# Performance work log

Measured on AMD Instinct MI355X. Metric: run time of the kernel, lower is better.

## Reference

```python
import jax, jax.numpy as jnp
import numpy as np

SCALE, Z, X, Y = 4, 9, 9, 9
INV_SQRT_2PI = 1.0 / np.sqrt(2.0 * np.pi)


def setup_inputs() -> dict:
    key = jax.random.key(0)
    k1, = jax.random.split(key, 1)
    inp = jax.random.normal(k1, (1, 1, 128, 512, 512), dtype=jnp.float32)
    return {
        "inp": inp,
        "mu_z": jnp.asarray(0.0, dtype=jnp.float32),
        "sig_z": jnp.asarray(0.1, dtype=jnp.float32),
        "bet_xy": jnp.asarray(2.0, dtype=jnp.float32),
        "bet_z": jnp.asarray(1.5, dtype=jnp.float32),
    }


def _gen_alf(bet_xy, bet_z):
    # squared distances along each axis; torch's loop overwrites the wrap-around
    # write, so the net result for odd sizes is simply (arange - size//2)**2
    zd = ((jnp.arange(Z) - Z // 2) ** 2).astype(jnp.float32)[:, None, None]
    xd = ((jnp.arange(X) - X // 2) ** 2).astype(jnp.float32)[None, :, None]
    yd = ((jnp.arange(Y) - Y // 2) ** 2).astype(jnp.float32)[None, None, :]
    d_2 = zd / bet_z ** 2 + (xd + yd) / bet_xy ** 2  # (Z, X, Y)
    return jnp.exp(-d_2 / 2) * INV_SQRT_2PI


def reference(inp, mu_z, sig_z, bet_xy, bet_z):
    z0 = jnp.exp(mu_z + 0.5 * sig_z ** 2)
    rec = inp * z0  # (N, 1, D, H, W)
    alf = _gen_alf(bet_xy, bet_z)[None, None]  # (1, 1, Z, X, Y)
    pad_z = (Z - SCALE + 1) // 2
    rec = jax.lax.conv_general_dilated(
        rec, alf,
        window_strides=(SCALE, 1, 1),
        padding=[(pad_z, pad_z), (X // 2, X // 2), (Y // 2, Y // 2)],
        dimension_numbers=("NCDHW", "OIDHW", "NCDHW"),
    )  # (N, 1, D//SCALE, H, W)
    rec = (rec - rec.min()) / (rec.max() - rec.min())
    return rec
```

## Files before the change

kernel.cpp:

```cpp
#include <hip/hip_runtime.h>

#define D_IN  128
#define D_OUT 32
#define H     512
#define W     512
#define W4    128
#define HB    16
#define ZR    (HB + 8)
#define NTHR  512

__global__ __launch_bounds__(NTHR)
void conv3d_fused(const float* __restrict__ inp, float* __restrict__ out,
                  const float* __restrict__ bxy_p, const float* __restrict__ bz_p,
                  float* __restrict__ blkMin, float* __restrict__ blkMax) {
    __shared__ float zbuf[ZR * W];
    __shared__ float hbuf[HB * W];

    const int d  = blockIdx.x >> 5;
    const int h0 = (blockIdx.x & 31) * HB;

    const float bz = bz_p[0], bx = bxy_p[0];
    const float iz = 1.0f / (2.0f * bz * bz);
    const float ix = 1.0f / (2.0f * bx * bx);
    float wz[9], wx[9];
#pragma unroll
    for (int k = 0; k < 9; ++k) {
        float dd = (float)(k - 4);
        wz[k] = expf(-dd * dd * iz);
        wx[k] = expf(-dd * dd * ix);
    }

    const float4* in4 = (const float4*)inp;
    float4* z4 = (float4*)zbuf;
    float4* h4 = (float4*)hbuf;

    for (int t = threadIdx.x; t < ZR * W4; t += NTHR) {
        int r  = t >> 7;
        int c4 = t & (W4 - 1);
        int h  = h0 - 4 + r;
        float4 acc = make_float4(0.f, 0.f, 0.f, 0.f);
        if ((unsigned)h < H) {
            int base = h * W4 + c4;
#pragma unroll
            for (int k = 0; k < 9; ++k) {
                int din = 4 * d - 3 + k;
                if ((unsigned)din < D_IN) {
                    float4 v = in4[din * (H * W4) + base];
                    acc.x += v.x * wz[k]; acc.y += v.y * wz[k];
                    acc.z += v.z * wz[k]; acc.w += v.w * wz[k];
                }
            }
        }
        z4[t] = acc;
    }
    __syncthreads();

    for (int t = threadIdx.x; t < HB * W4; t += NTHR) {
        int r  = t >> 7;
        int c4 = t & (W4 - 1);
        float4 acc = make_float4(0.f, 0.f, 0.f, 0.f);
#pragma unroll
        for (int k = 0; k < 9; ++k) {
            float4 v = z4[(r + k) * W4 + c4];
            acc.x += v.x * wx[k]; acc.y += v.y * wx[k];
            acc.z += v.z * wx[k]; acc.w += v.w * wx[k];
        }
        h4[t] = acc;
    }
    __syncthreads();

    float lmin =  3.402823466e38f;
    float lmax = -3.402823466e38f;
    float4* out4 = (float4*)out;
    for (int t = threadIdx.x; t < HB * W4; t += NTHR) {
        int r  = t >> 7;
        int c4 = t & (W4 - 1);
        float4 zv = make_float4(0.f, 0.f, 0.f, 0.f);
        float4 va = (c4 > 0)      ? h4[r * W4 + c4 - 1] : zv;
        float4 vb =                 h4[r * W4 + c4];
        float4 vc = (c4 < W4 - 1) ? h4[r * W4 + c4 + 1] : zv;
        float win[12] = {va.x, va.y, va.z, va.w,
                         vb.x, vb.y, vb.z, vb.w,
                         vc.x, vc.y, vc.z, vc.w};
        float4 o = make_float4(0.f, 0.f, 0.f, 0.f);
#pragma unroll
        for (int k = 0; k < 9; ++k) {
            o.x += win[k]     * wx[k];
            o.y += win[k + 1] * wx[k];
            o.z += win[k + 2] * wx[k];
            o.w += win[k + 3] * wx[k];
        }
        out4[(d * H + h0 + r) * W4 + c4] = o;
        lmin = fminf(lmin, fminf(fminf(o.x, o.y), fminf(o.z, o.w)));
        lmax = fmaxf(lmax, fmaxf(fmaxf(o.x, o.y), fmaxf(o.z, o.w)));
    }

#pragma unroll
    for (int off = 32; off > 0; off >>= 1) {
        lmin = fminf(lmin, __shfl_down(lmin, off, 64));
        lmax = fmaxf(lmax, __shfl_down(lmax, off, 64));
    }
    float* smin = &zbuf[0];
    float* smax = &zbuf[16];
    int lane = threadIdx.x & 63, wv = threadIdx.x >> 6;
    if (lane == 0) { smin[wv] = lmin; smax[wv] = lmax; }
    __syncthreads();
    if (threadIdx.x == 0) {
        float mn = smin[0], mx = smax[0];
#pragma unroll
        for (int i = 1; i < 8; ++i) { mn = fminf(mn, smin[i]); mx = fmaxf(mx, smax[i]); }
        blkMin[blockIdx.x] = mn;
        blkMax[blockIdx.x] = mx;
    }
}

__global__ void reduce_kernel(const float* __restrict__ blkMin, const float* __restrict__ blkMax,
                              float* __restrict__ fin, int nblk) {
    float lmin =  3.402823466e38f;
    float lmax = -3.402823466e38f;
    for (int i = threadIdx.x; i < nblk; i += blockDim.x) {
        lmin = fminf(lmin, blkMin[i]);
        lmax = fmaxf(lmax, blkMax[i]);
    }
#pragma unroll
    for (int off = 32; off > 0; off >>= 1) {
        lmin = fminf(lmin, __shfl_down(lmin, off, 64));
        lmax = fmaxf(lmax, __shfl_down(lmax, off, 64));
    }
    __shared__ float smin[4], smax[4];
    int lane = threadIdx.x & 63, wv = threadIdx.x >> 6;
    if (lane == 0) { smin[wv] = lmin; smax[wv] = lmax; }
    __syncthreads();
    if (threadIdx.x == 0) {
        fin[0] = fminf(fminf(smin[0], smin[1]), fminf(smin[2], smin[3]));
        fin[1] = fmaxf(fmaxf(smax[0], smax[1]), fmaxf(smax[2], smax[3]));
    }
}

__global__ void norm_kernel(const float* __restrict__ in, float* __restrict__ out,
                            const float* __restrict__ fin) {
    int tid = blockIdx.x * blockDim.x + threadIdx.x;
    float mn  = fin[0];
    float inv = 1.0f / (fin[1] - mn);
    float4 v = ((const float4*)in)[tid];
    ((float4*)out)[tid] = make_float4((v.x - mn) * inv, (v.y - mn) * inv,
                                      (v.z - mn) * inv, (v.w - mn) * inv);
}

extern "C" void kernel_launch(void* const* d_in, const int* in_sizes, int n_in,
                              void* d_out, int out_size, void* d_ws, size_t ws_size,
                              hipStream_t stream) {
    const float* inp    = (const float*)d_in[0];
    const float* bet_xy = (const float*)d_in[3];
    const float* bet_z  = (const float*)d_in[4];
    float* out = (float*)d_out;

    char* ws = (char*)d_ws;
    float* fin    = (float*)ws;
    float* blkMin = (float*)(ws + 4096);
    float* blkMax = (float*)(ws + 8192);
    float* bufA   = (float*)(ws + 65536);

    const int CONV_GRID = D_OUT * (H / HB);
    conv3d_fused<<<CONV_GRID, NTHR, 0, stream>>>(inp, bufA, bet_xy, bet_z, blkMin, blkMax);
    reduce_kernel<<<1, 256, 0, stream>>>(blkMin, blkMax, fin, CONV_GRID);

    const int NTASK = D_OUT * H * W4;
    norm_kernel<<<NTASK / 256, 256, 0, stream>>>(bufA, out, fin);
}
```

Before: 242.3 us.

## Split z-convolution into its own kernel and use atomic min/max reduction

The z-axis convolution becomes a separate elementwise kernel writing an intermediate buffer, so the HW conv kernel no longer recomputes the 9-tap z sum for its 8 halo rows on every block. The block height is halved and the separate reduce kernel is replaced by order-preserving uint atomicMin/atomicMax. Costs are an extra round trip of a 32 MB intermediate through global memory and one more launch, and the halo overhead ratio rises with the smaller tile.

```diff
diff --git a/kernel.cpp b/kernel.cpp
--- a/kernel.cpp
+++ b/kernel.cpp
@@ -5,57 +5,89 @@
 #define H     512
 #define W     512
 #define W4    128
-#define HB    16
+#define HB    8
 #define ZR    (HB + 8)
-#define NTHR  512
+#define K2THR 512
 
-__global__ __launch_bounds__(NTHR)
-void conv3d_fused(const float* __restrict__ inp, float* __restrict__ out,
-                  const float* __restrict__ bxy_p, const float* __restrict__ bz_p,
-                  float* __restrict__ blkMin, float* __restrict__ blkMax) {
-    __shared__ float zbuf[ZR * W];
-    __shared__ float hbuf[HB * W];
+__device__ __forceinline__ unsigned f2key(float f) {
+    unsigned u = __float_as_uint(f);
+    return (u & 0x80000000u) ? ~u : (u | 0x80000000u);
+}
+__device__ __forceinline__ float key2f(unsigned k) {
+    unsigned u = (k & 0x80000000u) ? (k ^ 0x80000000u) : ~k;
+    return __uint_as_float(u);
+}
 
-    const int d  = blockIdx.x >> 5;
-    const int h0 = (blockIdx.x & 31) * HB;
-
-    const float bz = bz_p[0], bx = bxy_p[0];
-    const float iz = 1.0f / (2.0f * bz * bz);
-    const float ix = 1.0f / (2.0f * bx * bx);
-    float wz[9], wx[9];
+__global__ void zconv_kernel(const float* __restrict__ inp, float* __restrict__ out,
+                             const float* __restrict__ bz_p, unsigned* __restrict__ fin_u) {
+    if (blockIdx.x == 0 && threadIdx.x == 0) {
+        fin_u[0] = 0xFFFFFFFFu;
+        fin_u[1] = 0u;
+    }
+    int tid = blockIdx.x * blockDim.x + threadIdx.x;
+    int w4 = tid & (W4 - 1);
+    int h  = (tid >> 7) & (H - 1);
+    int d  = tid >> 16;
+    float bz = bz_p[0];
+    float iz = 1.0f / (2.0f * bz * bz);
+    float wz[9];
 #pragma unroll
     for (int k = 0; k < 9; ++k) {
         float dd = (float)(k - 4);
         wz[k] = expf(-dd * dd * iz);
+    }
+    const float4* in4 = (const float4*)inp;
+    float4 acc = make_float4(0.f, 0.f, 0.f, 0.f);
+    int base = h * W4 + w4;
+#pragma unroll
+    for (int k = 0; k < 9; ++k) {
+        int din = 4 * d - 3 + k;
+        if ((unsigned)din < D_IN) {
+            float4 v = in4[din * (H * W4) + base];
+            acc.x += v.x * wz[k]; acc.y += v.y * wz[k];
+            acc.z += v.z * wz[k]; acc.w += v.w * wz[k];
+        }
+    }
+    ((float4*)out)[d * (H * W4) + base] = acc;
+}
+
+__global__ __launch_bounds__(K2THR)
+void hwconv_kernel(const float* __restrict__ in, float* __restrict__ out,
+                   const float* __restrict__ bxy_p, unsigned* __restrict__ fin_u) {
+    __shared__ float zbuf[ZR * W];
+    __shared__ float hbuf[HB * W];
+    __shared__ float smin[8], smax[8];
+
+    const int d  = blockIdx.x >> 6;
+    const int h0 = (blockIdx.x & 63) * HB;
+
+    float bx = bxy_p[0];
+    float ix = 1.0f / (2.0f * bx * bx);
+    float wx[9];
+#pragma unroll
+    for (int k = 0; k < 9; ++k) {
+        float dd = (float)(k - 4);
         wx[k] = expf(-dd * dd * ix);
     }
 
-    const float4* in4 = (const float4*)inp;
+    const float4* in4 = (const float4*)in;
     float4* z4 = (float4*)zbuf;
     float4* h4 = (float4*)hbuf;
 
-    for (int t = threadIdx.x; t < ZR * W4; t += NTHR) {
+#pragma unroll
+    for (int i = 0; i < (ZR * W4) / K2THR; ++i) {
+        int t  = threadIdx.x + i * K2THR;
         int r  = t >> 7;
         int c4 = t & (W4 - 1);
         int h  = h0 - 4 + r;
-        float4 acc = make_float4(0.f, 0.f, 0.f, 0.f);
-        if ((unsigned)h < H) {
-            int base = h * W4 + c4;
-#pragma unroll
-            for (int k = 0; k < 9; ++k) {
-                int din = 4 * d - 3 + k;
-                if ((unsigned)din < D_IN) {
-                    float4 v = in4[din * (H * W4) + base];
-                    acc.x += v.x * wz[k]; acc.y += v.y * wz[k];
-                    acc.z += v.z * wz[k]; acc.w += v.w * wz[k];
-                }
-            }
-        }
-        z4[t] = acc;
+        z4[t] = ((unsigned)h < H) ? in4[(d * H + h) * W4 + c4]
+                                  : make_float4(0.f, 0.f, 0.f, 0.f);
     }
     __syncthreads();
 
-    for (int t = threadIdx.x; t < HB * W4; t += NTHR) {
+#pragma unroll
+    for (int i = 0; i < (HB * W4) / K2THR; ++i) {
+        int t  = threadIdx.x + i * K2THR;
         int r  = t >> 7;
         int c4 = t & (W4 - 1);
         float4 acc = make_float4(0.f, 0.f, 0.f, 0.f);
@@ -72,7 +104,9 @@
     float lmin =  3.402823466e38f;
     float lmax = -3.402823466e38f;
     float4* out4 = (float4*)out;
-    for (int t = threadIdx.x; t < HB * W4; t += NTHR) {
+#pragma unroll
+    for (int i = 0; i < (HB * W4) / K2THR; ++i) {
+        int t  = threadIdx.x + i * K2THR;
         int r  = t >> 7;
         int c4 = t & (W4 - 1);
         float4 zv = make_float4(0.f, 0.f, 0.f, 0.f);
@@ -100,8 +134,6 @@
         lmin = fminf(lmin, __shfl_down(lmin, off, 64));
         lmax = fmaxf(lmax, __shfl_down(lmax, off, 64));
     }
-    float* smin = &zbuf[0];
-    float* smax = &zbuf[16];
     int lane = threadIdx.x & 63, wv = threadIdx.x >> 6;
     if (lane == 0) { smin[wv] = lmin; smax[wv] = lmax; }
     __syncthreads();
@@ -109,39 +141,17 @@
         float mn = smin[0], mx = smax[0];
 #pragma unroll
         for (int i = 1; i < 8; ++i) { mn = fminf(mn, smin[i]); mx = fmaxf(mx, smax[i]); }
-        blkMin[blockIdx.x] = mn;
-        blkMax[blockIdx.x] = mx;
-    }
-}
-
-__global__ void reduce_kernel(const float* __restrict__ blkMin, const float* __restrict__ blkMax,
-                              float* __restrict__ fin, int nblk) {
-    float lmin =  3.402823466e38f;
-    float lmax = -3.402823466e38f;
-    for (int i = threadIdx.x; i < nblk; i += blockDim.x) {
-        lmin = fminf(lmin, blkMin[i]);
-        lmax = fmaxf(lmax, blkMax[i]);
-    }
-#pragma unroll
-    for (int off = 32; off > 0; off >>= 1) {
-        lmin = fminf(lmin, __shfl_down(lmin, off, 64));
-        lmax = fmaxf(lmax, __shfl_down(lmax, off, 64));
-    }
-    __shared__ float smin[4], smax[4];
-    int lane = threadIdx.x & 63, wv = threadIdx.x >> 6;
-    if (lane == 0) { smin[wv] = lmin; smax[wv] = lmax; }
-    __syncthreads();
-    if (threadIdx.x == 0) {
-        fin[0] = fminf(fminf(smin[0], smin[1]), fminf(smin[2], smin[3]));
-        fin[1] = fmaxf(fmaxf(smax[0], smax[1]), fmaxf(smax[2], smax[3]));
+        atomicMin(&fin_u[0], f2key(mn));
+        atomicMax(&fin_u[1], f2key(mx));
     }
 }
 
 __global__ void norm_kernel(const float* __restrict__ in, float* __restrict__ out,
-                            const float* __restrict__ fin) {
+                            const unsigned* __restrict__ fin_u) {
     int tid = blockIdx.x * blockDim.x + threadIdx.x;
-    float mn  = fin[0];
-    float inv = 1.0f / (fin[1] - mn);
+    float mn  = key2f(fin_u[0]);
+    float mx  = key2f(fin_u[1]);
+    float inv = 1.0f / (mx - mn);
     float4 v = ((const float4*)in)[tid];
     ((float4*)out)[tid] = make_float4((v.x - mn) * inv, (v.y - mn) * inv,
                                       (v.z - mn) * inv, (v.w - mn) * inv);
@@ -156,15 +166,12 @@
     float* out = (float*)d_out;
 
     char* ws = (char*)d_ws;
-    float* fin    = (float*)ws;
-    float* blkMin = (float*)(ws + 4096);
-    float* blkMax = (float*)(ws + 8192);
-    float* bufA   = (float*)(ws + 65536);
-
-    const int CONV_GRID = D_OUT * (H / HB);
-    conv3d_fused<<<CONV_GRID, NTHR, 0, stream>>>(inp, bufA, bet_xy, bet_z, blkMin, blkMax);
-    reduce_kernel<<<1, 256, 0, stream>>>(blkMin, blkMax, fin, CONV_GRID);
+    unsigned* fin_u = (unsigned*)ws;
+    float* bufA = (float*)(ws + 65536);
+    float* bufB = (float*)(ws + 65536 + (size_t)33554432);
 
     const int NTASK = D_OUT * H * W4;
-    norm_kernel<<<NTASK / 256, 256, 0, stream>>>(bufA, out, fin);
+    zconv_kernel<<<NTASK / 256, 256, 0, stream>>>(inp, bufA, bet_z, fin_u);
+    hwconv_kernel<<<D_OUT * (H / HB), K2THR, 0, stream>>>(bufA, bufB, bet_xy, fin_u);
+    norm_kernel<<<NTASK / 256, 256, 0, stream>>>(bufB, out, fin_u);
 }
```

After: 269.4 us. 1.11x slower.
